# Performance work log

Hardware: AMD Instinct MI355X
Metric: run time of the kernel (lower is better)

Reference implementation:

```python
import jax, jax.numpy as jnp
import numpy as np

IOU_THRESHOLD = 0.1
EPS = 1e-7  # torchvision generalized_box_iou_loss eps


def _make_boxes(key, b, n, img=1000.0, wmin=10.0, wmax=120.0):
    k1, k2 = jax.random.split(key)
    cxy = jax.random.uniform(k1, (b, n, 2), jnp.float32, 0.0, img)
    wh = jax.random.uniform(k2, (b, n, 2), jnp.float32, wmin, wmax)
    return jnp.concatenate([cxy - 0.5 * wh, cxy + 0.5 * wh], axis=-1)  # xyxy


def setup_inputs() -> dict:
    key = jax.random.key(0)
    kp, kt = jax.random.split(key)
    pred_boxes = _make_boxes(kp, 16, 4096)    # [B, M, 4]
    target_boxes = _make_boxes(kt, 16, 512)   # [B, N, 4]
    return {"pred_boxes": pred_boxes, "target_boxes": target_boxes}


def _pairwise_iou(p, t):
    # p: [M,4], t: [N,4] xyxy -> [M,N]
    area_p = (p[:, 2] - p[:, 0]) * (p[:, 3] - p[:, 1])
    area_t = (t[:, 2] - t[:, 0]) * (t[:, 3] - t[:, 1])
    lt = jnp.maximum(p[:, None, :2], t[None, :, :2])
    rb = jnp.minimum(p[:, None, 2:], t[None, :, 2:])
    wh = jnp.clip(rb - lt, 0.0)
    inter = wh[..., 0] * wh[..., 1]
    union = area_p[:, None] + area_t[None, :] - inter
    return inter / union


def _greedy_match(iou):
    # Greedy: for each pred row (in order), take highest-IoU unused target with IoU > thr.
    N = iou.shape[1]
    def step(used, row):
        masked = jnp.where(used, -jnp.inf, row)  # [N]
        j = jnp.argmax(masked)
        valid = masked[j] > IOU_THRESHOLD
        used = used.at[j].set(used[j] | valid)
        return used, (j, valid)
    _, (idx, valid) = jax.lax.scan(step, jnp.zeros((N,), bool), iou)
    return idx, valid  # [M] int, [M] bool


def _giou_loss_pairs(p, t):
    # elementwise GIoU loss between p[i] and t[i]; p,t: [K,4] -> [K]
    x1 = jnp.maximum(p[:, 0], t[:, 0]); y1 = jnp.maximum(p[:, 1], t[:, 1])
    x2 = jnp.minimum(p[:, 2], t[:, 2]); y2 = jnp.minimum(p[:, 3], t[:, 3])
    inter = jnp.clip(x2 - x1, 0.0) * jnp.clip(y2 - y1, 0.0)
    area_p = (p[:, 2] - p[:, 0]) * (p[:, 3] - p[:, 1])
    area_t = (t[:, 2] - t[:, 0]) * (t[:, 3] - t[:, 1])
    union = area_p + area_t - inter
    iou = inter / (union + EPS)
    ex1 = jnp.minimum(p[:, 0], t[:, 0]); ey1 = jnp.minimum(p[:, 1], t[:, 1])
    ex2 = jnp.maximum(p[:, 2], t[:, 2]); ey2 = jnp.maximum(p[:, 3], t[:, 3])
    enc = (ex2 - ex1) * (ey2 - ey1)
    giou = iou - (enc - union) / (enc + EPS)
    return 1.0 - giou


def _image_loss(pred, tgt):
    # pred [M,4], tgt [N,4] with M != N -> greedy match then mean GIoU loss over matches
    iou = _pairwise_iou(pred, tgt)
    idx, valid = _greedy_match(iou)
    matched_t = tgt[idx]                    # [M,4]
    loss = _giou_loss_pairs(pred, matched_t)
    w = valid.astype(loss.dtype)
    cnt = w.sum()
    return jnp.where(cnt > 0, (loss * w).sum() / jnp.maximum(cnt, 1.0), 0.0)


def reference(pred_boxes, target_boxes):
    # batched path, reduction='mean': mean over per-image mean GIoU losses
    per_image = jax.vmap(_image_loss)(pred_boxes, target_boxes)  # [B]
    return per_image.mean()
```

## Files before the change

### kernel.cpp

```cpp
#include <hip/hip_runtime.h>
#include <math.h>

#define NB   16
#define NM   4096
#define NT   512
#define CAP  16
#define IOU_THR 0.1f
#define EPSG 1e-7f
#define NROWS (NB*NM)
#define T_WIN 1024
#define NWIN  (NM / T_WIN)
#define SENT  0xFFFFFFFFu

__global__ __launch_bounds__(256) void cand_kernel(
    const float4* __restrict__ pred, const float4* __restrict__ tgt,
    int* __restrict__ counts, float2* __restrict__ cands)
{
    __shared__ float4 t_lds[NT];
    const int rb = blockIdx.x * 64;
    const int b  = rb >> 12;
    for (int i = threadIdx.x; i < NT; i += 256)
        t_lds[i] = tgt[b * NT + i];
    __syncthreads();

    const int wv = threadIdx.x >> 6, lane = threadIdx.x & 63;
    const int row0 = rb + wv * 16;
    const unsigned long long lmask = (1ull << lane) - 1ull;

    float4 pa = pred[row0], pb = pred[row0 + 1];
    for (int rr = 0; rr < 16; rr += 2) {
        float4 p0 = pa, p1 = pb;
        if (rr + 2 < 16) {
            pa = pred[row0 + rr + 2];
            pb = pred[row0 + rr + 3];
        }
        float ap0 = (p0.z - p0.x) * (p0.w - p0.y);
        float ap1 = (p1.z - p1.x) * (p1.w - p1.y);
        int base0 = 0, base1 = 0;
        #pragma unroll
        for (int pass = 0; pass < NT / 64; ++pass) {
            int j = (pass << 6) + lane;
            float4 t = t_lds[j];
            float at = (t.z - t.x) * (t.w - t.y);
            float w0 = fmaxf(fminf(p0.z, t.z) - fmaxf(p0.x, t.x), 0.f);
            float h0 = fmaxf(fminf(p0.w, t.w) - fmaxf(p0.y, t.y), 0.f);
            float in0 = w0 * h0;
            float iou0 = in0 / ((ap0 + at) - in0);
            float w1 = fmaxf(fminf(p1.z, t.z) - fmaxf(p1.x, t.x), 0.f);
            float h1 = fmaxf(fminf(p1.w, t.w) - fmaxf(p1.y, t.y), 0.f);
            float in1 = w1 * h1;
            float iou1 = in1 / ((ap1 + at) - in1);
            bool q0 = iou0 > IOU_THR, q1 = iou1 > IOU_THR;
            unsigned long long m0 = __ballot(q0);
            unsigned long long m1 = __ballot(q1);
            if (q0) {
                int off = base0 + __popcll(m0 & lmask);
                if (off < CAP)
                    cands[(size_t)off * NROWS + row0 + rr] = make_float2(iou0, __int_as_float(j));
            }
            if (q1) {
                int off = base1 + __popcll(m1 & lmask);
                if (off < CAP)
                    cands[(size_t)off * NROWS + row0 + rr + 1] = make_float2(iou1, __int_as_float(j));
            }
            base0 += __popcll(m0);
            base1 += __popcll(m1);
        }
        if (lane == 0) {
            counts[row0 + rr]     = base0;
            counts[row0 + rr + 1] = base1;
        }
    }
}

__global__ __launch_bounds__(T_WIN) void win_auction(
    const float4* __restrict__ pred, const float4* __restrict__ tgt,
    const int* __restrict__ counts, const float2* __restrict__ cands,
    float* __restrict__ per_img)
{
    __shared__ float4   t_lds[NT];
    __shared__ unsigned claim[NT];
    __shared__ int lastprop;
    __shared__ unsigned char winovf[NWIN];
    __shared__ int ovf_min, ovf_res;
    __shared__ float rvv[T_WIN / 64];  __shared__ int rjj[T_WIN / 64];
    __shared__ float rls[T_WIN / 64];  __shared__ float rcs[T_WIN / 64];

    const int b = blockIdx.x, t = threadIdx.x, gbase = b * NM;
    const int wv = t >> 6, lane = t & 63;

    if (t < NT) {
        t_lds[t] = tgt[b * NT + t];
        claim[t] = SENT;
    }
    if (t < NWIN) winovf[t] = 0;
    if (t == 0) lastprop = -1;
    __syncthreads();

    int allCnt[NWIN];
    #pragma unroll
    for (int k = 0; k < NWIN; ++k) {
        allCnt[k] = counts[gbase + k * T_WIN + t];
        if (allCnt[k] > CAP) winovf[k] = 1;
    }
    float2 nC[CAP];
    #pragma unroll
    for (int e = 0; e < CAP; ++e) nC[e] = cands[(size_t)e * NROWS + gbase + t];
    __syncthreads();

    int rglob = 0;
    float2 cC[CAP];
    for (int w = 0; w < NWIN; ++w) {
        #pragma unroll
        for (int e = 0; e < CAP; ++e) cC[e] = nC[e];
        const int cCnt = allCnt[w];
        if (w + 1 < NWIN) {
            #pragma unroll
            for (int e = 0; e < CAP; ++e)
                nC[e] = cands[(size_t)e * NROWS + gbase + (w + 1) * T_WIN + t];
        }
        const unsigned row = (unsigned)(w * T_WIN + t);
        int  stt  = (cCnt > 0 && cCnt <= CAP) ? 0 : 2;
        int  myj  = -1;
        bool isovf = (cCnt > CAP);
        int  ovfj  = -1;

        for (;;) {
            for (;;) {
                if (stt == 1 && claim[myj] != row) stt = 0;
                bool did = false;
                if (stt == 0) {
                    for (int it = 0; it <= CAP; ++it) {
                        float bv = -1.f; int bj = -1;
                        #pragma unroll
                        for (int e = 0; e < CAP; ++e) {
                            float2 ce = cC[e];
                            int j = __float_as_int(ce.y) & (NT - 1);
                            unsigned cj = claim[j];
                            if (e < cCnt && cj >= row && ce.x > bv) { bv = ce.x; bj = j; }
                        }
                        if (bj < 0) { stt = 2; break; }
                        did = true;
                        unsigned old = atomicMin(&claim[bj], row);
                        if (old >= row) { myj = bj; stt = 1; break; }
                    }
                }
                if (did) lastprop = rglob;
                __syncthreads();
                int lp = lastprop;
                ++rglob;
                if (lp < rglob - 1) break;
            }
            if (!winovf[w]) break;
            if (t == 0) ovf_min = 0x7FFFFFFF;
            __syncthreads();
            bool pend = isovf && (ovfj < 0 || claim[ovfj] != row);
            if (pend) atomicMin(&ovf_min, (int)row);
            __syncthreads();
            const int rowF = ovf_min;
            if (rowF == 0x7FFFFFFF) break;
            {
                float4 p4 = pred[gbase + rowF];
                float v = -1.f; int bj = NT;
                if (t < NT) {
                    float4 tt = t_lds[t];
                    float area_p = (p4.z - p4.x) * (p4.w - p4.y);
                    float area_t = (tt.z - tt.x) * (tt.w - tt.y);
                    float wd = fmaxf(fminf(p4.z, tt.z) - fmaxf(p4.x, tt.x), 0.f);
                    float hd = fmaxf(fminf(p4.w, tt.w) - fmaxf(p4.y, tt.y), 0.f);
                    float inter = wd * hd;
                    float iou = inter / ((area_p + area_t) - inter);
                    bool freej = claim[t] > (unsigned)rowF;
                    v = freej ? iou : -1.f;
                    bj = freej ? t : NT;
                }
                #pragma unroll
                for (int off = 1; off < 64; off <<= 1) {
                    float ov = __shfl_xor(v, off);
                    int   oj = __shfl_xor(bj, off);
                    if (ov > v || (ov == v && oj < bj)) { v = ov; bj = oj; }
                }
                if (lane == 0) { rvv[wv] = v; rjj[wv] = bj; }
            }
            __syncthreads();
            if (t == 0) {
                float v = rvv[0]; int bj = rjj[0];
                for (int q = 1; q < T_WIN / 64; ++q)
                    if (rvv[q] > v || (rvv[q] == v && rjj[q] < bj)) { v = rvv[q]; bj = rjj[q]; }
                if (v > IOU_THR) { ovf_res = bj; claim[bj] = (unsigned)rowF; }
                else ovf_res = -1;
            }
            __syncthreads();
            if ((int)row == rowF) {
                if (ovf_res >= 0) ovfj = ovf_res;
                else isovf = false;
            }
        }
    }
    __syncthreads();

    float ls = 0.f, cs = 0.f;
    if (t < NT) {
        unsigned r = claim[t];
        if (r != SENT) {
            float4 p4 = pred[gbase + (int)r];
            float4 tt = t_lds[t];
            float inter = fmaxf(fminf(p4.z, tt.z) - fmaxf(p4.x, tt.x), 0.f) *
                          fmaxf(fminf(p4.w, tt.w) - fmaxf(p4.y, tt.y), 0.f);
            float area_p = (p4.z - p4.x) * (p4.w - p4.y);
            float area_t = (tt.z - tt.x) * (tt.w - tt.y);
            float uni = area_p + area_t - inter;
            float iou = inter / (uni + EPSG);
            float enc = (fmaxf(p4.z, tt.z) - fminf(p4.x, tt.x)) *
                        (fmaxf(p4.w, tt.w) - fminf(p4.y, tt.y));
            float giou = iou - (enc - uni) / (enc + EPSG);
            ls = 1.f - giou;
            cs = 1.f;
        }
    }
    #pragma unroll
    for (int off = 32; off >= 1; off >>= 1) {
        ls += __shfl_xor(ls, off);
        cs += __shfl_xor(cs, off);
    }
    if (lane == 0) { rls[wv] = ls; rcs[wv] = cs; }
    __syncthreads();
    if (t == 0) {
        float L = 0.f, C = 0.f;
        for (int q = 0; q < T_WIN / 64; ++q) { L += rls[q]; C += rcs[q]; }
        per_img[b] = (C > 0.f) ? L / C : 0.f;
    }
}

__global__ void reduce_kernel(const float* __restrict__ per_img,
                              float* __restrict__ out)
{
    if (threadIdx.x == 0 && blockIdx.x == 0) {
        float s = 0.f;
        for (int i = 0; i < NB; ++i) s += per_img[i];
        out[0] = s / (float)NB;
    }
}

extern "C" void kernel_launch(void* const* d_in, const int* in_sizes, int n_in,
                              void* d_out, int out_size, void* d_ws, size_t ws_size,
                              hipStream_t stream)
{
    const float4* pred = (const float4*)d_in[0];
    const float4* tgt  = (const float4*)d_in[1];

    char* ws = (char*)d_ws;
    int*    counts  = (int*)ws;
    size_t  off1    = (size_t)NROWS * sizeof(int);
    float2* cands   = (float2*)(ws + off1);
    size_t  off2    = off1 + (size_t)CAP * NROWS * sizeof(float2);
    float*  per_img = (float*)(ws + off2);

    cand_kernel<<<NROWS / 64, 256, 0, stream>>>(pred, tgt, counts, cands);
    win_auction<<<NB, T_WIN, 0, stream>>>(pred, tgt, counts, cands, per_img);
    reduce_kernel<<<1, 64, 0, stream>>>(per_img, (float*)d_out);
}
```

Before: 64.30 us.

## Fuse candidate, auction and reduce kernels into one launch with per-image spin sync

Merges the candidate-generation, per-image auction and final reduction kernels into one kernel of 256 blocks. Each block first produces candidates for 256 rows, then signals a per-image atomic counter. The first block of each image spin-waits until all 16 producer blocks for that image finish, then runs the auction, and a last-block atomic counter performs the final mean. This removes two kernel launches and their gaps, but adds a memset, spin-waiting that depends on all producer blocks being co-resident or scheduled, and 1024-thread blocks for the candidate phase.

```diff
diff --git a/kernel.cpp b/kernel.cpp
--- a/kernel.cpp
+++ b/kernel.cpp
@@ -8,99 +8,99 @@
 #define IOU_THR 0.1f
 #define EPSG 1e-7f
 #define NROWS (NB*NM)
-#define T_WIN 1024
-#define NWIN  (NM / T_WIN)
+#define T_BLK 1024
+#define NWIN  (NM / T_BLK)
+#define PB_ROWS 256
 #define SENT  0xFFFFFFFFu
 
-__global__ __launch_bounds__(256) void cand_kernel(
+__global__ __launch_bounds__(T_BLK) void fused_kernel(
     const float4* __restrict__ pred, const float4* __restrict__ tgt,
-    int* __restrict__ counts, float2* __restrict__ cands)
-{
-    __shared__ float4 t_lds[NT];
-    const int rb = blockIdx.x * 64;
-    const int b  = rb >> 12;
-    for (int i = threadIdx.x; i < NT; i += 256)
-        t_lds[i] = tgt[b * NT + i];
-    __syncthreads();
-
-    const int wv = threadIdx.x >> 6, lane = threadIdx.x & 63;
-    const int row0 = rb + wv * 16;
-    const unsigned long long lmask = (1ull << lane) - 1ull;
-
-    float4 pa = pred[row0], pb = pred[row0 + 1];
-    for (int rr = 0; rr < 16; rr += 2) {
-        float4 p0 = pa, p1 = pb;
-        if (rr + 2 < 16) {
-            pa = pred[row0 + rr + 2];
-            pb = pred[row0 + rr + 3];
-        }
-        float ap0 = (p0.z - p0.x) * (p0.w - p0.y);
-        float ap1 = (p1.z - p1.x) * (p1.w - p1.y);
-        int base0 = 0, base1 = 0;
-        #pragma unroll
-        for (int pass = 0; pass < NT / 64; ++pass) {
-            int j = (pass << 6) + lane;
-            float4 t = t_lds[j];
-            float at = (t.z - t.x) * (t.w - t.y);
-            float w0 = fmaxf(fminf(p0.z, t.z) - fmaxf(p0.x, t.x), 0.f);
-            float h0 = fmaxf(fminf(p0.w, t.w) - fmaxf(p0.y, t.y), 0.f);
-            float in0 = w0 * h0;
-            float iou0 = in0 / ((ap0 + at) - in0);
-            float w1 = fmaxf(fminf(p1.z, t.z) - fmaxf(p1.x, t.x), 0.f);
-            float h1 = fmaxf(fminf(p1.w, t.w) - fmaxf(p1.y, t.y), 0.f);
-            float in1 = w1 * h1;
-            float iou1 = in1 / ((ap1 + at) - in1);
-            bool q0 = iou0 > IOU_THR, q1 = iou1 > IOU_THR;
-            unsigned long long m0 = __ballot(q0);
-            unsigned long long m1 = __ballot(q1);
-            if (q0) {
-                int off = base0 + __popcll(m0 & lmask);
-                if (off < CAP)
-                    cands[(size_t)off * NROWS + row0 + rr] = make_float2(iou0, __int_as_float(j));
-            }
-            if (q1) {
-                int off = base1 + __popcll(m1 & lmask);
-                if (off < CAP)
-                    cands[(size_t)off * NROWS + row0 + rr + 1] = make_float2(iou1, __int_as_float(j));
-            }
-            base0 += __popcll(m0);
-            base1 += __popcll(m1);
-        }
-        if (lane == 0) {
-            counts[row0 + rr]     = base0;
-            counts[row0 + rr + 1] = base1;
-        }
-    }
-}
-
-__global__ __launch_bounds__(T_WIN) void win_auction(
-    const float4* __restrict__ pred, const float4* __restrict__ tgt,
-    const int* __restrict__ counts, const float2* __restrict__ cands,
-    float* __restrict__ per_img)
+    int* __restrict__ counts, float2* __restrict__ cands,
+    int* __restrict__ prod_done, float* __restrict__ per_img,
+    int* __restrict__ done_ctr, float* __restrict__ out)
 {
     __shared__ float4   t_lds[NT];
     __shared__ unsigned claim[NT];
     __shared__ int lastprop;
     __shared__ unsigned char winovf[NWIN];
     __shared__ int ovf_min, ovf_res;
-    __shared__ float rvv[T_WIN / 64];  __shared__ int rjj[T_WIN / 64];
-    __shared__ float rls[T_WIN / 64];  __shared__ float rcs[T_WIN / 64];
-
-    const int b = blockIdx.x, t = threadIdx.x, gbase = b * NM;
-    const int wv = t >> 6, lane = t & 63;
-
-    if (t < NT) {
-        t_lds[t] = tgt[b * NT + t];
-        claim[t] = SENT;
-    }
+    __shared__ float rvv[T_BLK / 64];  __shared__ int rjj[T_BLK / 64];
+    __shared__ float rls[T_BLK / 64];  __shared__ float rcs[T_BLK / 64];
+
+    const int blk = blockIdx.x, t = threadIdx.x;
+    const int b   = blk >> 4;
+    const int wv  = t >> 6, lane = t & 63;
+
+    if (t < NT) t_lds[t] = tgt[b * NT + t];
+    __syncthreads();
+
+    {
+        const int row0 = blk * PB_ROWS + wv * 16;
+        const unsigned long long lmask = (1ull << lane) - 1ull;
+        float4 pa = pred[row0], pb = pred[row0 + 1];
+        for (int rr = 0; rr < 16; rr += 2) {
+            float4 p0 = pa, p1 = pb;
+            if (rr + 2 < 16) { pa = pred[row0 + rr + 2]; pb = pred[row0 + rr + 3]; }
+            float ap0 = (p0.z - p0.x) * (p0.w - p0.y);
+            float ap1 = (p1.z - p1.x) * (p1.w - p1.y);
+            int base0 = 0, base1 = 0;
+            #pragma unroll
+            for (int pass = 0; pass < NT / 64; ++pass) {
+                int j = (pass << 6) + lane;
+                float4 tb = t_lds[j];
+                float at = (tb.z - tb.x) * (tb.w - tb.y);
+                float w0 = fmaxf(fminf(p0.z, tb.z) - fmaxf(p0.x, tb.x), 0.f);
+                float h0 = fmaxf(fminf(p0.w, tb.w) - fmaxf(p0.y, tb.y), 0.f);
+                float in0 = w0 * h0;
+                float iou0 = in0 / ((ap0 + at) - in0);
+                float w1 = fmaxf(fminf(p1.z, tb.z) - fmaxf(p1.x, tb.x), 0.f);
+                float h1 = fmaxf(fminf(p1.w, tb.w) - fmaxf(p1.y, tb.y), 0.f);
+                float in1 = w1 * h1;
+                float iou1 = in1 / ((ap1 + at) - in1);
+                bool q0 = iou0 > IOU_THR, q1 = iou1 > IOU_THR;
+                unsigned long long m0 = __ballot(q0), m1 = __ballot(q1);
+                if (q0) {
+                    int off = base0 + __popcll(m0 & lmask);
+                    if (off < CAP)
+                        cands[(size_t)off * NROWS + row0 + rr]     = make_float2(iou0, __int_as_float(j));
+                }
+                if (q1) {
+                    int off = base1 + __popcll(m1 & lmask);
+                    if (off < CAP)
+                        cands[(size_t)off * NROWS + row0 + rr + 1] = make_float2(iou1, __int_as_float(j));
+                }
+                base0 += __popcll(m0);
+                base1 += __popcll(m1);
+            }
+            if (lane == 0) {
+                counts[row0 + rr]     = base0;
+                counts[row0 + rr + 1] = base1;
+            }
+        }
+    }
+    __syncthreads();
+    if (t == 0) {
+        __threadfence();
+        atomicAdd(&prod_done[b], 1);
+    }
+
+    if ((blk & 15) != 0) return;
+
+    if (t < NT) claim[t] = SENT;
     if (t < NWIN) winovf[t] = 0;
-    if (t == 0) lastprop = -1;
-    __syncthreads();
-
+    if (t == 0) {
+        lastprop = -1;
+        while (__hip_atomic_load(&prod_done[b], __ATOMIC_ACQUIRE,
+                                 __HIP_MEMORY_SCOPE_AGENT) < 16) {}
+        __threadfence();
+    }
+    __syncthreads();
+
+    const int gbase = b * NM;
     int allCnt[NWIN];
     #pragma unroll
     for (int k = 0; k < NWIN; ++k) {
-        allCnt[k] = counts[gbase + k * T_WIN + t];
+        allCnt[k] = counts[gbase + k * T_BLK + t];
         if (allCnt[k] > CAP) winovf[k] = 1;
     }
     float2 nC[CAP];
@@ -117,9 +117,9 @@
         if (w + 1 < NWIN) {
             #pragma unroll
             for (int e = 0; e < CAP; ++e)
-                nC[e] = cands[(size_t)e * NROWS + gbase + (w + 1) * T_WIN + t];
-        }
-        const unsigned row = (unsigned)(w * T_WIN + t);
+                nC[e] = cands[(size_t)e * NROWS + gbase + (w + 1) * T_BLK + t];
+        }
+        const unsigned row = (unsigned)(w * T_BLK + t);
         int  stt  = (cCnt > 0 && cCnt <= CAP) ? 0 : 2;
         int  myj  = -1;
         bool isovf = (cCnt > CAP);
@@ -185,7 +185,7 @@
             __syncthreads();
             if (t == 0) {
                 float v = rvv[0]; int bj = rjj[0];
-                for (int q = 1; q < T_WIN / 64; ++q)
+                for (int q = 1; q < T_BLK / 64; ++q)
                     if (rvv[q] > v || (rvv[q] == v && rjj[q] < bj)) { v = rvv[q]; bj = rjj[q]; }
                 if (v > IOU_THR) { ovf_res = bj; claim[bj] = (unsigned)rowF; }
                 else ovf_res = -1;
@@ -227,18 +227,17 @@
     __syncthreads();
     if (t == 0) {
         float L = 0.f, C = 0.f;
-        for (int q = 0; q < T_WIN / 64; ++q) { L += rls[q]; C += rcs[q]; }
+        for (int q = 0; q < T_BLK / 64; ++q) { L += rls[q]; C += rcs[q]; }
         per_img[b] = (C > 0.f) ? L / C : 0.f;
-    }
-}
-
-__global__ void reduce_kernel(const float* __restrict__ per_img,
-                              float* __restrict__ out)
-{
-    if (threadIdx.x == 0 && blockIdx.x == 0) {
-        float s = 0.f;
-        for (int i = 0; i < NB; ++i) s += per_img[i];
-        out[0] = s / (float)NB;
+        __threadfence();
+        int ret = atomicAdd(done_ctr, 1);
+        if (ret == NB - 1) {
+            __threadfence();
+            volatile float* vp = per_img;
+            float s = 0.f;
+            for (int i = 0; i < NB; ++i) s += vp[i];
+            out[0] = s / (float)NB;
+        }
     }
 }
 
@@ -255,8 +254,11 @@
     float2* cands   = (float2*)(ws + off1);
     size_t  off2    = off1 + (size_t)CAP * NROWS * sizeof(float2);
     float*  per_img = (float*)(ws + off2);
-
-    cand_kernel<<<NROWS / 64, 256, 0, stream>>>(pred, tgt, counts, cands);
-    win_auction<<<NB, T_WIN, 0, stream>>>(pred, tgt, counts, cands, per_img);
-    reduce_kernel<<<1, 64, 0, stream>>>(per_img, (float*)d_out);
+    size_t  off3    = off2 + 64;
+    int*    done_ctr  = (int*)(ws + off3);
+    int*    prod_done = done_ctr + 1;
+
+    hipMemsetAsync(done_ctr, 0, (NB + 1) * sizeof(int), stream);
+    fused_kernel<<<NROWS / PB_ROWS, T_BLK, 0, stream>>>(
+        pred, tgt, counts, cands, prod_done, per_img, done_ctr, (float*)d_out);
 }
```

After: 78.11 us. 21.5% more time.
